# Kernel tuning notes

Measured on AMD Instinct MI355X. Metric: run time of the kernel, lower is better.

The kernel has to match this reference:

```python
import jax, jax.numpy as jnp
import numpy as np

# hypercfg constants (init_kwargs)
AUX = 0.05
L1W = 5.0
VPW = 1.0
VNW = 1.0


def _lsa_square(cost):
    """Jonker-Volgenant shortest-augmenting-path Hungarian on a square numpy
    cost matrix. Returns rows[j] = row assigned to column j. Runs on host,
    mirroring the original CPU scipy.optimize.linear_sum_assignment call."""
    n = cost.shape[0]
    INF = np.inf
    u = np.zeros(n + 1)
    v = np.zeros(n + 1)
    p = np.zeros(n + 1, dtype=np.int64)   # p[j] = row matched to column j (1-indexed)
    way = np.zeros(n + 1, dtype=np.int64)
    for i in range(1, n + 1):
        p[0] = i
        j0 = 0
        minv = np.full(n + 1, INF)
        used = np.zeros(n + 1, dtype=bool)
        while True:
            used[j0] = True
            i0 = p[j0]
            cur = cost[i0 - 1, :] - u[i0] - v[1:]
            free = ~used[1:]
            upd = free & (cur < minv[1:])
            minv1 = minv[1:]
            minv1[upd] = cur[upd]
            way1 = way[1:]
            way1[upd] = j0
            mfree = np.where(free, minv1, INF)
            j1 = int(np.argmin(mfree)) + 1
            delta = mfree[j1 - 1]
            used_idx = np.nonzero(used)[0]
            u[p[used_idx]] += delta
            v[used_idx] -= delta
            minv1[free] -= delta
            j0 = j1
            if p[j0] == 0:
                break
        while j0 != 0:
            j1 = way[j0]
            p[j0] = p[j1]
            j0 = j1
    return p[1:] - 1


def _match(cost_mk):
    """Rectangular assignment, cost [M, K] with K <= M: pad with a constant
    column block (dummy columns cost the same for any row, so the real K
    columns get the optimal assignment, matching scipy on rectangles)."""
    M, K = cost_mk.shape
    pad = np.zeros((M, M), dtype=np.float64)
    pad[:, :K] = cost_mk
    rows = _lsa_square(pad)
    return rows[:K]


def _cost(meta_points, meta_visibles, gtpoints, gtvisibles):
    # meta_points: [S,B,L,M,2]  gtpoints: [S,B,K,2]
    # meta_visibles: [S,B,M,1]  gtvisibles: [S,B,K,1]
    S, B, L, M, _ = meta_points.shape
    # pairwise L1 cost: [S,B,L,M,K]
    diff = jnp.abs(meta_points[:, :, :, :, None, :] - gtpoints[:, :, None, None, :, :]).sum(-1)
    # delta[l] = L - (l+1), per-layer slack (torch.linspace(1, L, L))
    delta = (L - jnp.arange(1, L + 1, dtype=meta_points.dtype)) * AUX
    cost_p_ml = jax.nn.relu(diff - delta[None, None, :, None, None])
    gtv = gtvisibles[:, :, :, 0][:, :, None, :]          # [S,B,1,K]
    cost_p = gtv * cost_p_ml.mean(2)                     # [S,B,M,K]
    cost_vp = -gtv * jnp.log(meta_visibles)              # [S,B,M,1] -> [S,B,M,K]
    cost_vn = -(1.0 - gtv) * jnp.log(1.0 - meta_visibles)
    cost = L1W * cost_p + VPW * cost_vp + VNW * cost_vn  # [S,B,M,K]
    return cost.mean(0)                                  # mean over shots -> [B,M,K]


def setup_inputs() -> dict:
    key = jax.random.key(0)
    ks = jax.random.split(key, 5)
    S, B, L, M, K = 6, 16, 8, 256, 128
    meta_points = jax.random.uniform(ks[0], (S, B, L, M, 2), dtype=jnp.float32)
    # keep probabilities strictly inside (0,1) so log() is finite
    meta_visibles = jax.random.uniform(ks[1], (S, B, M, 1), dtype=jnp.float32) * 0.9 + 0.05
    covisibles = jax.random.uniform(ks[2], (B, K), dtype=jnp.float32)
    gtpoints = jax.random.uniform(ks[3], (S, B, K, 2), dtype=jnp.float32)
    gtvisibles = (jax.random.uniform(ks[4], (S, B, K, 1)) > 0.5).astype(jnp.float32)
    return {
        "meta_points": meta_points,
        "meta_visibles": meta_visibles,
        "covisibles": covisibles,
        "gtpoints": gtpoints,
        "gtvisibles": gtvisibles,
    }


def reference(meta_points, meta_visibles, covisibles, gtpoints, gtvisibles):
    # covisibles only provides the batch size in the original module
    cost = np.asarray(jax.jit(_cost)(meta_points, meta_visibles, gtpoints, gtvisibles))
    bs = cost.shape[0]
    # per-batch Hungarian on host (sequential data-dependent algorithm);
    # result[b, k] = meta index matched to keypoint k (already kp-sorted,
    # matching the argsort-reorder in the torch code)
    out = np.stack([_match(cost[b]) for b in range(bs)])
    return jnp.asarray(out, dtype=jnp.int64)
```

## Files before the change

kernel.cpp:

```cpp
#include <hip/hip_runtime.h>
#include <math.h>


#define S_ 6
#define B_ 16
#define L_ 8
#define M_ 256
#define K_ 128

__global__ void cost_kernel(const float* __restrict__ mp,
                            const float* __restrict__ mv,
                            const float* __restrict__ gt,
                            const float* __restrict__ gv,
                            float* __restrict__ cost)
{
#pragma clang fp contract(off)
    const int b = blockIdx.x;
    const int m = blockIdx.y;
    const int k = threadIdx.x;

    float accS = 0.0f;
    for (int s = 0; s < S_; ++s) {
        const int sb = s * B_ + b;
        const float gx = gt[(sb * K_ + k) * 2 + 0];
        const float gy = gt[(sb * K_ + k) * 2 + 1];
        float accL = 0.0f;
#pragma unroll
        for (int l = 0; l < L_; ++l) {
            const int base = ((sb * L_ + l) * M_ + m) * 2;
            const float dx = fabsf(mp[base + 0] - gx);
            const float dy = fabsf(mp[base + 1] - gy);
            const float diff = dx + dy;
            const float dl = (float)(L_ - (l + 1)) * 0.05f;
            const float t = diff - dl;
            accL += fmaxf(t, 0.0f);
        }
        const float meanL = accL * 0.125f;
        const float mvv = mv[sb * M_ + m];
        const float gtv = gv[sb * K_ + k];
        const float lp = -logf(mvv);
        const float ln = -logf(1.0f - mvv);
        const float val = (gtv != 0.0f) ? (5.0f * meanL + lp) : ln;
        accS += val;
    }
    cost[(b * M_ + m) * K_ + k] = accS * (1.0f / 6.0f);
}

__device__ __forceinline__ double bits2d(int lo, int hi) {
    const unsigned long long u =
        ((unsigned long long)(unsigned)hi << 32) | (unsigned)lo;
    return __longlong_as_double((long long)u);
}
__device__ __forceinline__ void d2bits(double d, int& lo, int& hi) {
    const unsigned long long u = (unsigned long long)__double_as_longlong(d);
    lo = (int)(u & 0xffffffffull);
    hi = (int)(u >> 32);
}
__device__ __forceinline__ double readlane_d(double d, int l) {
    int lo, hi; d2bits(d, lo, hi);
    return bits2d(__builtin_amdgcn_readlane(lo, l),
                  __builtin_amdgcn_readlane(hi, l));
}

#define RSTG(LOV, HIV, FOP, CTRL, RM)                                            \
    {                                                                            \
        const int nlo_ = __builtin_amdgcn_update_dpp(LOV, LOV, CTRL, RM, 0xf, false); \
        const int nhi_ = __builtin_amdgcn_update_dpp(HIV, HIV, CTRL, RM, 0xf, false); \
        const double r_ = FOP(bits2d(LOV, HIV), bits2d(nlo_, nhi_));             \
        d2bits(r_, LOV, HIV);                                                    \
    }
#define RLADDER(LOV, HIV, FOP)                                                   \
    RSTG(LOV, HIV, FOP, 0x111, 0xf)                              \
    RSTG(LOV, HIV, FOP, 0x112, 0xf)                              \
    RSTG(LOV, HIV, FOP, 0x114, 0xf)                              \
    RSTG(LOV, HIV, FOP, 0x118, 0xf)                              \
    RSTG(LOV, HIV, FOP, 0x142, 0xa)                \
    RSTG(LOV, HIV, FOP, 0x143, 0xc)

#define SELBEST(EXJ1, EXJ2, JOUT, VOUT, UOUT)                                    \
    {                                                                            \
        const double vm2_ = ((used & 4) || (jd2 == (EXJ1)) || (jd2 == (EXJ2)))   \
                                ? NINF : v2;                                     \
        const double vm3_ = ((used & 8) || (jd3 == (EXJ1)) || (jd3 == (EXJ2)))   \
                                ? NINF : v3;                                     \
        const double bx_ = fmax(vm2_, vm3_);                                     \
        int xlo_, xhi_; d2bits(bx_, xlo_, xhi_);                                 \
        RLADDER(xlo_, xhi_, fmax)                                                \
        VOUT = bits2d(__builtin_amdgcn_readlane(xlo_, 63),                       \
                      __builtin_amdgcn_readlane(xhi_, 63));                      \
        int jc_ = BIG;                                                           \
        if (vm3_ == VOUT) jc_ = jd3;                                             \
        if (vm2_ == VOUT) jc_ = jd2;               \
        const unsigned long long bd_ = __ballot(jc_ != BIG);                     \
        JOUT = __builtin_amdgcn_readlane(jc_, (int)__builtin_ctzll(bd_));        \
        const int ol_ = ((JOUT) - 129) >> 1, sl_ = ((JOUT) - 129) & 1;           \
        UOUT = readlane_d(sl_ ? up3 : up2, ol_);                                 \
    }

__global__ __launch_bounds__(64, 1) void match_kernel(const float* __restrict__ cost,
                                                      int* __restrict__ out)
{
#pragma clang fp contract(off)
    const int b = blockIdx.x;
    const int lane = threadIdx.x;
    const float* C = cost + (size_t)b * M_ * K_;
    const double INF = __builtin_inf();
    const double NINF = -__builtin_inf();
    const int BIG = 0x7fffffff;

    __shared__ float  C_lds[M_ * K_];
    __shared__ double u_lds[257];
    __shared__ int    p_lds[257];
    __shared__ double vd_lds[128];
    __shared__ double Dcons[128];
    __shared__ int    clog[128];

    for (int t = lane; t < (M_ * K_) / 4; t += 64)
        ((float4*)C_lds)[t] = ((const float4*)C)[t];

    for (int t = lane; t < 257; t += 64) {
        u_lds[t] = 0.0;
        p_lds[t] = (t >= 129) ? (t - 128) : 0;
    }
    for (int t = lane; t < 128; t += 64) vd_lds[t] = 0.0;
    __syncthreads();

    double v0 = 0.0, v1 = 0.0;
    const int jd2 = 2 * lane + 129;
    const int jd3 = 2 * lane + 130;

    for (int i = 129; i <= 256; ++i) {
        const int pj0 = p_lds[2 * lane + 1];
        const int pj1 = p_lds[2 * lane + 2];
        double ur0 = u_lds[pj0], ur1 = u_lds[pj1];
        const double up0 = ur0, up1 = ur1;
        const double up2 = u_lds[2 * lane + 1];
        const double up3 = u_lds[2 * lane + 2];
        const double v2 = vd_lds[2 * lane];
        const double v3 = vd_lds[2 * lane + 1];

        float2 cc = *(const float2*)(C_lds + (i - 1) * K_ + 2 * lane);
        double u_i0 = 0.0;
        int used = 0;
        double usum = 0.0;
        int j1 = 0;
        int ptr = 0;

        int jdH, jdQ, jdN; double vdH, vdQ, vdN, udH, udQ, udN;
        SELBEST(-1, -1, jdH, vdH, udH)
        SELBEST(jdH, -1, jdQ, vdQ, udQ)
        float2 ccH = *(const float2*)(C_lds + (jdH - 129) * K_ + 2 * lane);
        float2 ccQ = *(const float2*)(C_lds + (jdQ - 129) * K_ + 2 * lane);
        double dval = (0.0 - u_i0) - vdH;

        for (;;) {
            double cd0 = ((double)cc.x - u_i0) - v0;
            double cd1 = ((double)cc.y - u_i0) - v1;
            if (used & 1) cd0 = INF;
            if (used & 2) cd1 = INF;
            double bv = fmin(cd0, cd1);
            int lo, hi; d2bits(bv, lo, hi);
            RLADDER(lo, hi, fmin)
            const double rmin = bits2d(__builtin_amdgcn_readlane(lo, 63),
                                       __builtin_amdgcn_readlane(hi, 63));

            SELBEST(jdH, jdQ, jdN, vdN, udN)
            const float2 ccN = *(const float2*)(C_lds + (jdN - 129) * K_ + 2 * lane);

            if (rmin <= dval) {
                const double delta = rmin;
                usum += delta;
                if (used & 1) { ur0 += delta; v0 -= delta; }
                if (used & 2) { ur1 += delta; v1 -= delta; }

                int jr = BIG;
                if (cd1 == delta) jr = 2 * lane + 2;
                if (cd0 == delta) jr = 2 * lane + 1;
                const unsigned long long br = __ballot(jr != BIG);
                j1 = __builtin_amdgcn_readlane(jr, (int)__builtin_ctzll(br));

                const int ol = (j1 - 1) >> 1, sl = (j1 - 1) & 1;
                const int psel = sl ? pj1 : pj0;
                const int i0n = __builtin_amdgcn_readlane(psel, ol);
                if (i0n == 0) break;

                const double u_n = readlane_d(sl ? up1 : up0, ol);
                if (lane == ol) used |= (1 << sl);
                u_i0 = u_n;
                cc = *(const float2*)(C_lds + (i0n - 1) * K_ + 2 * lane);
                dval = (0.0 - u_i0) - vdH;
            } else {
                const double delta = dval;
                usum += delta;
                if (used & 1) { ur0 += delta; v0 -= delta; }
                if (used & 2) { ur1 += delta; v1 -= delta; }
                if (lane == 0) { clog[ptr] = jdH; Dcons[ptr] = usum; }
                ++ptr;
                const int olc = (jdH - 129) >> 1, slc = (jdH - 129) & 1;
                if (lane == olc) used |= (4 << slc);
                j1 = jdH;
                u_i0 = udH;
                cc = ccH;
                jdH = jdQ; vdH = vdQ; udH = udQ; ccH = ccQ;
                jdQ = jdN; vdQ = vdN; udQ = udN; ccQ = ccN;
                dval = (0.0 - u_i0) - vdH;
            }
        }

        __syncthreads();
        if (used & 1) u_lds[pj0] = ur0;
        if (used & 2) u_lds[pj1] = ur1;
        {
            const int t0 = 2 * lane, t1 = 2 * lane + 1;
            if (t0 < ptr) {
                const int j = clog[t0];
                const double amt = usum - Dcons[t0];
                u_lds[j - 128] += amt;
                vd_lds[j - 129] -= amt;
            }
            if (t1 < ptr) {
                const int j = clog[t1];
                const double amt = usum - Dcons[t1];
                u_lds[j - 128] += amt;
                vd_lds[j - 129] -= amt;
            }
        }
        if (lane == 0) { p_lds[j1] = i; u_lds[i] = usum; }
        __syncthreads();
    }

    for (int j = lane; j < K_; j += 64)
        out[b * K_ + j] = p_lds[j + 1] - 1;
}

extern "C" void kernel_launch(void* const* d_in, const int* in_sizes, int n_in,
                              void* d_out, int out_size, void* d_ws, size_t ws_size,
                              hipStream_t stream) {
    const float* mp = (const float*)d_in[0];
    const float* mv = (const float*)d_in[1];
    const float* gt = (const float*)d_in[3];
    const float* gv = (const float*)d_in[4];
    int* out = (int*)d_out;
    float* cost = (float*)d_ws;

    dim3 gridA(B_, M_);
    cost_kernel<<<gridA, K_, 0, stream>>>(mp, mv, gt, gv, cost);
    match_kernel<<<B_, 64, 0, stream>>>(cost, out);
}
```

Baseline: 1.644 ms.

## Cache per-row minimum reduced cost to skip wave-wide reductions in Hungarian search

Precomputes, for every cost row, the minimum reduced cost over real columns and its argmin, stored in LDS. The shortest-path loop then uses this cached value instead of a full DPP reduction whenever the cached column has not become used during the current augmentation. The cache is repaired after each augmentation by rescanning rows whose argmin column's potential changed and relaxing against columns whose potential dropped. The lookahead SELBEST is also moved off the hot path into the dummy-column branch. This adds per-iteration maintenance work and extra synchronisation, and the cached tie-breaking and exactness must match the original argmin.

New measurement: 5.120 ms. +211.5%, slower.

```diff
diff --git a/kernel.cpp b/kernel.cpp
--- a/kernel.cpp
+++ b/kernel.cpp
@@ -77,12 +77,17 @@
     RSTG(LOV, HIV, FOP, 0x142, 0xa)                \
     RSTG(LOV, HIV, FOP, 0x143, 0xc)
 
-#define SELBEST(EXJ1, EXJ2, JOUT, VOUT, UOUT)                                    \
+#define FSTG(W, CTRL, RM)                                                        \
     {                                                                            \
-        const double vm2_ = ((used & 4) || (jd2 == (EXJ1)) || (jd2 == (EXJ2)))   \
-                                ? NINF : v2;                                     \
-        const double vm3_ = ((used & 8) || (jd3 == (EXJ1)) || (jd3 == (EXJ2)))   \
-                                ? NINF : v3;                                     \
+        const int nw_ = __builtin_amdgcn_update_dpp(W, W, CTRL, RM, 0xf, false); \
+        const float f_ = fminf(__int_as_float(W), __int_as_float(nw_));          \
+        W = __float_as_int(f_);                                                  \
+    }
+
+#define SELBEST(EXJ1, JOUT, VOUT, UOUT)                                          \
+    {                                                                            \
+        const double vm2_ = ((used & 4) || (jd2 == (EXJ1))) ? NINF : v2;         \
+        const double vm3_ = ((used & 8) || (jd3 == (EXJ1))) ? NINF : v3;         \
         const double bx_ = fmax(vm2_, vm3_);                                     \
         int xlo_, xhi_; d2bits(bx_, xlo_, xhi_);                                 \
         RLADDER(xlo_, xhi_, fmax)                                                \
@@ -112,12 +117,13 @@
     __shared__ double u_lds[257];
     __shared__ int    p_lds[257];
     __shared__ double vd_lds[128];
+    __shared__ double cmin_lds[256];
+    __shared__ int    cjmin_lds[256];
     __shared__ double Dcons[128];
     __shared__ int    clog[128];
 
     for (int t = lane; t < (M_ * K_) / 4; t += 64)
         ((float4*)C_lds)[t] = ((const float4*)C)[t];
-
     for (int t = lane; t < 257; t += 64) {
         u_lds[t] = 0.0;
         p_lds[t] = (t >= 129) ? (t - 128) : 0;
@@ -125,6 +131,21 @@
     for (int t = lane; t < 128; t += 64) vd_lds[t] = 0.0;
     __syncthreads();
 
+    for (int r = 0; r < 256; ++r) {
+        const float a  = C_lds[r * K_ + lane];
+        const float c2 = C_lds[r * K_ + 64 + lane];
+        int w = __float_as_int(fminf(a, c2));
+        FSTG(w, 0x111, 0xf) FSTG(w, 0x112, 0xf) FSTG(w, 0x114, 0xf)
+        FSTG(w, 0x118, 0xf) FSTG(w, 0x142, 0xa) FSTG(w, 0x143, 0xc)
+        const float mval = __int_as_float(__builtin_amdgcn_readlane(w, 63));
+        const unsigned long long ba = __ballot(a == mval);
+        const unsigned long long bb = __ballot(c2 == mval);
+        const int col = ba ? (int)__builtin_ctzll(ba)
+                           : 64 + (int)__builtin_ctzll(bb);
+        if (lane == 0) { cmin_lds[r] = (double)mval; cjmin_lds[r] = col + 1; }
+    }
+    __syncthreads();
+
     double v0 = 0.0, v1 = 0.0;
     const int jd2 = 2 * lane + 129;
     const int jd3 = 2 * lane + 130;
@@ -132,100 +153,186 @@
     for (int i = 129; i <= 256; ++i) {
         const int pj0 = p_lds[2 * lane + 1];
         const int pj1 = p_lds[2 * lane + 2];
-        double ur0 = u_lds[pj0], ur1 = u_lds[pj1];
-        const double up0 = ur0, up1 = ur1;
+        const double up0 = u_lds[pj0], up1 = u_lds[pj1];
         const double up2 = u_lds[2 * lane + 1];
         const double up3 = u_lds[2 * lane + 2];
         const double v2 = vd_lds[2 * lane];
         const double v3 = vd_lds[2 * lane + 1];
 
-        float2 cc = *(const float2*)(C_lds + (i - 1) * K_ + 2 * lane);
         double u_i0 = 0.0;
         int used = 0;
         double usum = 0.0;
+        double Ua0 = 0.0, Ua1 = 0.0;
         int j1 = 0;
         int ptr = 0;
-
-        int jdH, jdQ, jdN; double vdH, vdQ, vdN, udH, udQ, udN;
-        SELBEST(-1, -1, jdH, vdH, udH)
-        SELBEST(jdH, -1, jdQ, vdQ, udQ)
-        float2 ccH = *(const float2*)(C_lds + (jdH - 129) * K_ + 2 * lane);
-        float2 ccQ = *(const float2*)(C_lds + (jdQ - 129) * K_ + 2 * lane);
-        double dval = (0.0 - u_i0) - vdH;
+        int jU0 = 0, jU1 = 0, jU2 = 0, jU3 = 0, nU = 0;
+
+        int jdH, jdQ; double vdH, vdQ, udH, udQ;
+        SELBEST(-1, jdH, vdH, udH)
+        SELBEST(jdH, jdQ, vdQ, udQ)
+        double cmH = cmin_lds[jdH - 129]; int cjH = cjmin_lds[jdH - 129];
+        double cmQ = cmin_lds[jdQ - 129]; int cjQ = cjmin_lds[jdQ - 129];
+
+        int r0 = i - 1;
+        double cmC = cmin_lds[r0]; int cjC = cjmin_lds[r0];
 
         for (;;) {
-            double cd0 = ((double)cc.x - u_i0) - v0;
-            double cd1 = ((double)cc.y - u_i0) - v1;
-            if (used & 1) cd0 = INF;
-            if (used & 2) cd1 = INF;
-            double bv = fmin(cd0, cd1);
-            int lo, hi; d2bits(bv, lo, hi);
-            RLADDER(lo, hi, fmin)
-            const double rmin = bits2d(__builtin_amdgcn_readlane(lo, 63),
-                                       __builtin_amdgcn_readlane(hi, 63));
-
-            SELBEST(jdH, jdQ, jdN, vdN, udN)
-            const float2 ccN = *(const float2*)(C_lds + (jdN - 129) * K_ + 2 * lane);
+            const double dval = (0.0 - u_i0) - vdH;
+            double rmin; int rj = 0;
+            const bool cached_ok = (nU < 5) && (cjC != jU0) && (cjC != jU1)
+                                            && (cjC != jU2) && (cjC != jU3);
+            if (cached_ok) {
+                rmin = cmC - u_i0;
+                rj = cjC;
+            } else {
+                double cd0 = ((double)C_lds[r0 * K_ + 2 * lane] - u_i0) - v0;
+                double cd1 = ((double)C_lds[r0 * K_ + 2 * lane + 1] - u_i0) - v1;
+                if (used & 1) cd0 = INF;
+                if (used & 2) cd1 = INF;
+                double bv = fmin(cd0, cd1);
+                int lo, hi; d2bits(bv, lo, hi);
+                RLADDER(lo, hi, fmin)
+                rmin = bits2d(__builtin_amdgcn_readlane(lo, 63),
+                              __builtin_amdgcn_readlane(hi, 63));
+                int jr = BIG;
+                if (cd1 == rmin) jr = 2 * lane + 2;
+                if (cd0 == rmin) jr = 2 * lane + 1;
+                const unsigned long long br = __ballot(jr != BIG);
+                if (br) rj = __builtin_amdgcn_readlane(jr, (int)__builtin_ctzll(br));
+            }
 
             if (rmin <= dval) {
                 const double delta = rmin;
                 usum += delta;
-                if (used & 1) { ur0 += delta; v0 -= delta; }
-                if (used & 2) { ur1 += delta; v1 -= delta; }
-
-                int jr = BIG;
-                if (cd1 == delta) jr = 2 * lane + 2;
-                if (cd0 == delta) jr = 2 * lane + 1;
-                const unsigned long long br = __ballot(jr != BIG);
-                j1 = __builtin_amdgcn_readlane(jr, (int)__builtin_ctzll(br));
-
+                j1 = rj;
                 const int ol = (j1 - 1) >> 1, sl = (j1 - 1) & 1;
-                const int psel = sl ? pj1 : pj0;
-                const int i0n = __builtin_amdgcn_readlane(psel, ol);
+                const int i0n = __builtin_amdgcn_readlane(sl ? pj1 : pj0, ol);
                 if (i0n == 0) break;
-
                 const double u_n = readlane_d(sl ? up1 : up0, ol);
-                if (lane == ol) used |= (1 << sl);
+                if (lane == ol) {
+                    used |= (1 << sl);
+                    if (sl == 0) Ua0 = usum; else Ua1 = usum;
+                }
+                if (nU == 0) jU0 = j1; else if (nU == 1) jU1 = j1;
+                else if (nU == 2) jU2 = j1; else if (nU == 3) jU3 = j1;
+                ++nU;
                 u_i0 = u_n;
-                cc = *(const float2*)(C_lds + (i0n - 1) * K_ + 2 * lane);
-                dval = (0.0 - u_i0) - vdH;
+                r0 = i0n - 1;
+                cmC = cmin_lds[r0]; cjC = cjmin_lds[r0];
             } else {
                 const double delta = dval;
                 usum += delta;
-                if (used & 1) { ur0 += delta; v0 -= delta; }
-                if (used & 2) { ur1 += delta; v1 -= delta; }
                 if (lane == 0) { clog[ptr] = jdH; Dcons[ptr] = usum; }
-                ++ptr;
                 const int olc = (jdH - 129) >> 1, slc = (jdH - 129) & 1;
                 if (lane == olc) used |= (4 << slc);
-                j1 = jdH;
+                ++ptr;
                 u_i0 = udH;
-                cc = ccH;
-                jdH = jdQ; vdH = vdQ; udH = udQ; ccH = ccQ;
-                jdQ = jdN; vdQ = vdN; udQ = udN; ccQ = ccN;
-                dval = (0.0 - u_i0) - vdH;
+                r0 = jdH - 129;
+                cmC = cmH; cjC = cjH;
+                jdH = jdQ; vdH = vdQ; udH = udQ; cmH = cmQ; cjH = cjQ;
+                int jdN; double vdN, udN;
+                SELBEST(jdH, jdN, vdN, udN)
+                jdQ = jdN; vdQ = vdN; udQ = udN;
+                cmQ = cmin_lds[jdQ - 129]; cjQ = cjmin_lds[jdQ - 129];
             }
         }
 
         __syncthreads();
-        if (used & 1) u_lds[pj0] = ur0;
-        if (used & 2) u_lds[pj1] = ur1;
-        {
-            const int t0 = 2 * lane, t1 = 2 * lane + 1;
-            if (t0 < ptr) {
-                const int j = clog[t0];
-                const double amt = usum - Dcons[t0];
-                u_lds[j - 128] += amt;
-                vd_lds[j - 129] -= amt;
-            }
-            if (t1 < ptr) {
-                const int j = clog[t1];
-                const double amt = usum - Dcons[t1];
-                u_lds[j - 128] += amt;
-                vd_lds[j - 129] -= amt;
-            }
+        if (used & 1) { const double a = usum - Ua0; u_lds[pj0] = up0 + a; v0 -= a; }
+        if (used & 2) { const double a = usum - Ua1; u_lds[pj1] = up1 + a; v1 -= a; }
+        if (lane < ptr) {
+            const int j = clog[lane];
+            const double amt = usum - Dcons[lane];
+            u_lds[j - 128] += amt;
+            vd_lds[j - 129] -= amt;
+        }
+        if (lane + 64 < ptr) {
+            const int j = clog[lane + 64];
+            const double amt = usum - Dcons[lane + 64];
+            u_lds[j - 128] += amt;
+            vd_lds[j - 129] -= amt;
         }
         if (lane == 0) { p_lds[j1] = i; u_lds[i] = usum; }
+        __syncthreads();
+
+        if (nU > 0) {
+            int cjs[4], ubs[4];
+#pragma unroll
+            for (int g = 0; g < 4; ++g) cjs[g] = cjmin_lds[lane + 64 * g];
+#pragma unroll
+            for (int g = 0; g < 4; ++g) {
+                const int ow = (cjs[g] - 1) >> 1;
+                ubs[g] = __builtin_amdgcn_ds_bpermute(ow << 2, used);
+            }
+#pragma unroll
+            for (int g = 0; g < 4; ++g) {
+                const int sb = (cjs[g] - 1) & 1;
+                const bool flag = ((ubs[g] >> sb) & 1) != 0;
+                unsigned long long fb = __ballot(flag);
+                while (fb) {
+                    const int ln = (int)__builtin_ctzll(fb);
+                    fb &= fb - 1;
+                    const int rr = ln + 64 * g;
+                    const double c0 = (double)C_lds[rr * K_ + 2 * lane] - v0;
+                    const double c1 = (double)C_lds[rr * K_ + 2 * lane + 1] - v1;
+                    double bv2 = fmin(c0, c1);
+                    int lo, hi; d2bits(bv2, lo, hi);
+                    RLADDER(lo, hi, fmin)
+                    const double m = bits2d(__builtin_amdgcn_readlane(lo, 63),
+                                            __builtin_amdgcn_readlane(hi, 63));
+                    int jr = BIG;
+                    if (c1 == m) jr = 2 * lane + 2;
+                    if (c0 == m) jr = 2 * lane + 1;
+                    const unsigned long long brr = __ballot(jr != BIG);
+                    const int jsel =
+                        __builtin_amdgcn_readlane(jr, (int)__builtin_ctzll(brr));
+                    if (lane == 0) { cmin_lds[rr] = m; cjmin_lds[rr] = jsel; }
+                }
+            }
+        }
+        __syncthreads();
+
+        if (nU > 0) {
+            double cmr[4]; int cjr[4];
+#pragma unroll
+            for (int g = 0; g < 4; ++g) {
+                cmr[g] = cmin_lds[lane + 64 * g];
+                cjr[g] = cjmin_lds[lane + 64 * g];
+            }
+            unsigned long long m0 = __ballot((used & 1) != 0);
+            unsigned long long m1 = __ballot((used & 2) != 0);
+            while (m0) {
+                const int ol = (int)__builtin_ctzll(m0); m0 &= m0 - 1;
+                const int j = 2 * ol + 1;
+                const double va = readlane_d(v0, ol);
+#pragma unroll
+                for (int g = 0; g < 4; ++g) {
+                    const double cnd =
+                        (double)C_lds[(lane + 64 * g) * K_ + (j - 1)] - va;
+                    if (cnd < cmr[g] || (cnd == cmr[g] && j < cjr[g])) {
+                        cmr[g] = cnd; cjr[g] = j;
+                    }
+                }
+            }
+            while (m1) {
+                const int ol = (int)__builtin_ctzll(m1); m1 &= m1 - 1;
+                const int j = 2 * ol + 2;
+                const double va = readlane_d(v1, ol);
+#pragma unroll
+                for (int g = 0; g < 4; ++g) {
+                    const double cnd =
+                        (double)C_lds[(lane + 64 * g) * K_ + (j - 1)] - va;
+                    if (cnd < cmr[g] || (cnd == cmr[g] && j < cjr[g])) {
+                        cmr[g] = cnd; cjr[g] = j;
+                    }
+                }
+            }
+#pragma unroll
+            for (int g = 0; g < 4; ++g) {
+                cmin_lds[lane + 64 * g] = cmr[g];
+                cjmin_lds[lane + 64 * g] = cjr[g];
+            }
+        }
         __syncthreads();
     }
 
```
